# Kernel tuning notes

Measured on AMD Instinct MI355X. Metric: run time of the kernel, lower is better.

The kernel has to match this reference:

```python
import jax, jax.numpy as jnp
import numpy as np

B, S, E, H, D, R = 2, 2048, 1024, 16, 64, 16


def setup_inputs() -> dict:
    key = jax.random.key(0)
    ks = jax.random.split(key, 9)
    s = lambda k, shape, fan: jax.random.normal(k, shape, dtype=jnp.float32) / np.sqrt(fan)
    return {
        "x": jax.random.normal(ks[0], (B, S, E), dtype=jnp.float32),
        "Wq": s(ks[1], (H, E, D), E),
        "bq": jnp.zeros((H, D), jnp.float32),
        "Wk": s(ks[2], (H, E, D), E),
        "bk": jnp.zeros((H, D), jnp.float32),
        "Wvd": s(ks[3], (H, E, R), E),
        "bvd": jnp.zeros((H, R), jnp.float32),
        "Wvu": s(ks[4], (H, R, D), R),
        "bvu": jnp.zeros((H, D), jnp.float32),
    }


def reference(x, Wq, bq, Wk, bk, Wvd, bvd, Wvu, bvu):
    b, s, e = x.shape
    # per-head projections, vectorized over heads h
    q = jnp.einsum('bse,hed->bhsd', x, Wq) + bq[None, :, None, :]
    k = jnp.einsum('bse,hed->bhsd', x, Wk) + bk[None, :, None, :]
    # NOTE: original scales by sqrt(embedding_dimension), not head dim
    scores = jnp.einsum('bhsd,bhtd->bhst', q, k) / jnp.sqrt(jnp.float32(e))
    # original mask: masked_fill where key_idx < query_idx (anti-causal)
    qi = jnp.arange(s)[:, None]
    ki = jnp.arange(s)[None, :]
    scores = jnp.where(ki < qi, -jnp.inf, scores)
    att = jax.nn.softmax(scores, axis=-1)  # dropout p=0 (eval)
    # low-rank value: up(down(x))
    vd = jnp.einsum('bse,her->bhsr', x, Wvd) + bvd[None, :, None, :]
    v = jnp.einsum('bhsr,hrd->bhsd', vd, Wvu) + bvu[None, :, None, :]
    out = jnp.einsum('bhst,bhtd->bhsd', att, v)
    # concat heads along last dim (head order = stack order)
    return out.transpose(0, 2, 1, 3).reshape(b, s, -1)
```

## Files before the change

kernel.cpp:

```cpp
#include <hip/hip_runtime.h>
#include <stdint.h>

#define B_ 2
#define S_ 2048
#define E_ 1024
#define H_ 16
#define D_ 64
#define R_ 16

typedef short s16x8 __attribute__((ext_vector_type(8)));
typedef short s16x4 __attribute__((ext_vector_type(4)));
typedef float f32x4 __attribute__((ext_vector_type(4)));

__device__ __forceinline__ unsigned short f2bf(float f) {
  union { float f; unsigned u; } v; v.f = f;
  return (unsigned short)((v.u + 0x8000u) >> 16);
}

__device__ __forceinline__ void load_lds16(const void* g, void* l) {
  __builtin_amdgcn_global_load_lds(
      (__attribute__((address_space(1))) void*)(g),
      (__attribute__((address_space(3))) void*)(l), 16, 0, 0);
}


__global__ void k_cvt_x(const float* __restrict__ x, unsigned short* __restrict__ xb) {
  int i = (blockIdx.x * 256 + threadIdx.x) * 4;
  float4 v = *(const float4*)(x + i);
  ushort4 o;
  o.x = f2bf(v.x); o.y = f2bf(v.y); o.z = f2bf(v.z); o.w = f2bf(v.w);
  *(ushort4*)(xb + i) = o;
}

__global__ void k_prep_wqk(const float* __restrict__ Wq, const float* __restrict__ Wk,
                           unsigned short* __restrict__ Wt) {
  __shared__ float T[64][65];
  const int t = threadIdx.x;
  const int which = blockIdx.x >> 8;
  const int h = (blockIdx.x >> 4) & 15;
  const int et = blockIdx.x & 15;
  const float* src = (which ? Wk : Wq) + (h * E_ + et * 64) * D_;
#pragma unroll
  for (int pr = 0; pr < 4; ++pr) {
    const int row = pr * 16 + (t >> 4);
    const int col = (t & 15) * 4;
    float4 v = *(const float4*)(src + row * 64 + col);
    T[row][col] = v.x; T[row][col + 1] = v.y; T[row][col + 2] = v.z; T[row][col + 3] = v.w;
  }
  __syncthreads();
#pragma unroll
  for (int pr = 0; pr < 4; ++pr) {
    const int d = pr * 16 + (t >> 4);
    const int ec = (t & 15) * 4;
    ushort4 o;
    o.x = f2bf(T[ec][d]); o.y = f2bf(T[ec + 1][d]);
    o.z = f2bf(T[ec + 2][d]); o.w = f2bf(T[ec + 3][d]);
    *(ushort4*)(Wt + ((which << 10) + h * 64 + d) * 1024 + et * 64 + ec) = o;
  }
}

__global__ void k_prep_wv(const float* __restrict__ Wvd, const float* __restrict__ Wvu,
                          unsigned short* __restrict__ Wt) {
  const int idx = blockIdx.x * 256 + threadIdx.x;
  const int row = idx >> 10;
  const int e = idx & 1023;
  const int h = row >> 6, d = row & 63;
  const float4* wd4 = (const float4*)(Wvd + (h << 14) + e * 16);
  const float* wu = Wvu + h * R_ * D_ + d;
  float acc = 0.f;
#pragma unroll
  for (int r4 = 0; r4 < 4; ++r4) {
    float4 a = wd4[r4];
    acc += a.x * wu[(r4 * 4 + 0) * 64];
    acc += a.y * wu[(r4 * 4 + 1) * 64];
    acc += a.z * wu[(r4 * 4 + 2) * 64];
    acc += a.w * wu[(r4 * 4 + 3) * 64];
  }
  Wt[(2048 + row) * 1024 + e] = f2bf(acc);
}

__global__ void k_prep_b(const float* __restrict__ bq, const float* __restrict__ bk,
                         const float* __restrict__ bvd, const float* __restrict__ Wvu,
                         const float* __restrict__ bvu, float* __restrict__ ball) {
  int n = blockIdx.x * 256 + threadIdx.x;
  int which = n >> 10;
  int hd = n & 1023;
  int h = hd >> 6, d = hd & 63;
  float v;
  if (which == 0) v = bq[hd];
  else if (which == 1) v = bk[hd];
  else {
    v = bvu[hd];
#pragma unroll
    for (int r = 0; r < R_; ++r) v += bvd[h * R_ + r] * Wvu[(h * R_ + r) * D_ + d];
  }
  ball[n] = v;
}


__global__ __launch_bounds__(256, 2) void k_gemm_qkv(
    const unsigned short* __restrict__ X, const unsigned short* __restrict__ Wt,
    const float* __restrict__ ball,
    unsigned short* __restrict__ Qb, unsigned short* __restrict__ Kb,
    unsigned short* __restrict__ Vb) {
  __shared__ unsigned short As[128 * 32];
  __shared__ unsigned short Bs[128 * 32];
  const int tid = threadIdx.x;
  const int lane = tid & 63, wave = tid >> 6;
  const int quad = lane >> 4, l16 = lane & 15;
  const int mBase = blockIdx.y * 128, nBase = blockIdx.x * 128;
  const int wm = (wave & 1) * 64, wn = (wave >> 1) * 64;
  const int lrow = lane >> 2, lcol = (lane & 3) * 8;

  f32x4 acc[4][4];
#pragma unroll
  for (int mi = 0; mi < 4; ++mi)
#pragma unroll
    for (int ni = 0; ni < 4; ++ni) acc[mi][ni] = (f32x4){0.f, 0.f, 0.f, 0.f};

  for (int k0 = 0; k0 < E_; k0 += 32) {
#pragma unroll
    for (int i = 0; i < 2; ++i) {
      const int r0 = __builtin_amdgcn_readfirstlane((wave + i * 4) * 16);
      load_lds16(X + (mBase + r0 + lrow) * E_ + k0 + lcol, &As[r0 * 32]);
      load_lds16(Wt + (nBase + r0 + lrow) * E_ + k0 + lcol, &Bs[r0 * 32]);
    }
    __syncthreads();
    s16x8 af[4], bfr[4];
#pragma unroll
    for (int mi = 0; mi < 4; ++mi)
      af[mi] = *(const s16x8*)&As[(wm + mi * 16 + l16) * 32 + quad * 8];
#pragma unroll
    for (int ni = 0; ni < 4; ++ni)
      bfr[ni] = *(const s16x8*)&Bs[(wn + ni * 16 + l16) * 32 + quad * 8];
#pragma unroll
    for (int mi = 0; mi < 4; ++mi)
#pragma unroll
      for (int ni = 0; ni < 4; ++ni)
        acc[mi][ni] = __builtin_amdgcn_mfma_f32_16x16x32_bf16(af[mi], bfr[ni], acc[mi][ni], 0, 0, 0);
    __syncthreads();
  }

  const int which = nBase >> 10;
#pragma unroll
  for (int ni = 0; ni < 4; ++ni) {
    const int n = nBase + wn + ni * 16 + l16;
    const int nh = n & 1023;
    const int h = nh >> 6, d = nh & 63;
    const float bias = ball[n];
#pragma unroll
    for (int mi = 0; mi < 4; ++mi) {
      const int m0 = mBase + wm + mi * 16 + quad * 4;
      const int b = m0 >> 11;
      const int s = m0 & 2047;
      const int bh = b * H_ + h;
      if (which == 2) {
        ushort4 pk;
        pk.x = f2bf(acc[mi][ni][0] + bias);
        pk.y = f2bf(acc[mi][ni][1] + bias);
        pk.z = f2bf(acc[mi][ni][2] + bias);
        pk.w = f2bf(acc[mi][ni][3] + bias);
        *(ushort4*)(Vb + (bh * D_ + d) * S_ + s) = pk;
      } else {
        unsigned short* dst = (which == 0 ? Qb : Kb) + (bh * S_ + s) * D_ + d;
#pragma unroll
        for (int r = 0; r < 4; ++r) dst[r * D_] = f2bf(acc[mi][ni][r] + bias);
      }
    }
  }
}


__global__ __launch_bounds__(256, 2) void k_attn(
    const unsigned short* __restrict__ Qb, const unsigned short* __restrict__ Kb,
    const unsigned short* __restrict__ Vb, float* __restrict__ out) {
  __shared__ unsigned short Ks[2 * 64 * 32];
  __shared__ unsigned short Vs[2 * 64 * 32];
  __shared__ unsigned short Ps[4 * 2 * 16 * 36];
  const int tid = threadIdx.x;
  const int lane = tid & 63, wave = tid >> 6;
  const int quad = lane >> 4, l16 = lane & 15;
  const int bh = blockIdx.x & 31;
  const int qt = blockIdx.x >> 5;
  const int q0 = qt * 64;
  const int lrow = lane >> 2, lcol = (lane & 3) * 8;
  const float K1 = 1.44269504f / 32.f;
  const float K0 = -28.8539008f;

  s16x8 qf[2];
  {
    const unsigned short* qp = Qb + (bh * S_ + q0 + wave * 16 + l16) * D_ + quad * 8;
    qf[0] = *(const s16x8*)qp;
    qf[1] = *(const s16x8*)(qp + 32);
  }
  f32x4 o[4];
#pragma unroll
  for (int dc = 0; dc < 4; ++dc) o[dc] = (f32x4){0.f, 0.f, 0.f, 0.f};
  float l_acc[4] = {0.f, 0.f, 0.f, 0.f};

  unsigned short* myPs = &Ps[wave * 1152];

  for (int kt = qt; kt < S_ / 64; ++kt) {
    const int k0 = kt * 64;
    const int r0 = __builtin_amdgcn_readfirstlane(wave * 16);
#pragma unroll
    for (int hdc = 0; hdc < 2; ++hdc) {
      load_lds16(Kb + (bh * S_ + k0 + r0 + lrow) * D_ + hdc * 32 + lcol,
                 &Ks[hdc * 2048 + r0 * 32]);
      load_lds16(Vb + (bh * D_ + r0 + lrow) * S_ + k0 + hdc * 32 + lcol,
                 &Vs[hdc * 2048 + r0 * 32]);
    }
    __syncthreads();

    f32x4 sc[4];
#pragma unroll
    for (int tc = 0; tc < 4; ++tc) {
      f32x4 a = (f32x4){0.f, 0.f, 0.f, 0.f};
#pragma unroll
      for (int dc = 0; dc < 2; ++dc) {
        s16x8 kb = *(const s16x8*)&Ks[dc * 2048 + (tc * 16 + l16) * 32 + quad * 8];
        a = __builtin_amdgcn_mfma_f32_16x16x32_bf16(qf[dc], kb, a, 0, 0, 0);
      }
      sc[tc] = a;
    }

    if (kt == qt) {
#pragma unroll
      for (int tc = 0; tc < 4; ++tc)
#pragma unroll
        for (int r = 0; r < 4; ++r) {
          const int t = tc * 16 + l16;
          const int q = wave * 16 + quad * 4 + r;
          if (t < q) sc[tc][r] = -3.0e38f;
        }
    }

#pragma unroll
    for (int tc = 0; tc < 4; ++tc)
#pragma unroll
      for (int r = 0; r < 4; ++r) {
        float p = exp2f(fmaf(sc[tc][r], K1, K0));
        l_acc[r] += p;
        myPs[(tc >> 1) * 576 + (quad * 4 + r) * 36 + (tc & 1) * 16 + l16] = f2bf(p);
      }

#pragma unroll
    for (int dc = 0; dc < 4; ++dc) {
#pragma unroll
      for (int kc = 0; kc < 2; ++kc) {
        s16x4 plo = *(const s16x4*)&myPs[kc * 576 + l16 * 36 + quad * 8];
        s16x4 phi = *(const s16x4*)&myPs[kc * 576 + l16 * 36 + quad * 8 + 4];
        s16x8 pf = __builtin_shufflevector(plo, phi, 0, 1, 2, 3, 4, 5, 6, 7);
        s16x8 vb = *(const s16x8*)&Vs[kc * 2048 + (dc * 16 + l16) * 32 + quad * 8];
        o[dc] = __builtin_amdgcn_mfma_f32_16x16x32_bf16(pf, vb, o[dc], 0, 0, 0);
      }
    }
    __syncthreads();
  }

#pragma unroll
  for (int off = 1; off < 16; off <<= 1)
#pragma unroll
    for (int r = 0; r < 4; ++r) l_acc[r] += __shfl_xor(l_acc[r], off);
  float rinv[4];
#pragma unroll
  for (int r = 0; r < 4; ++r) rinv[r] = 1.f / l_acc[r];

  const int b = bh >> 4, h = bh & 15;
#pragma unroll
  for (int dc = 0; dc < 4; ++dc)
#pragma unroll
    for (int r = 0; r < 4; ++r) {
      const int s = q0 + wave * 16 + quad * 4 + r;
      out[(b * S_ + s) * (H_ * D_) + h * D_ + dc * 16 + l16] = o[dc][r] * rinv[r];
    }
}


extern "C" void kernel_launch(void* const* d_in, const int* in_sizes, int n_in,
                              void* d_out, int out_size, void* d_ws, size_t ws_size,
                              hipStream_t stream) {
  const float* x   = (const float*)d_in[0];
  const float* Wq  = (const float*)d_in[1];
  const float* bq  = (const float*)d_in[2];
  const float* Wk  = (const float*)d_in[3];
  const float* bk  = (const float*)d_in[4];
  const float* Wvd = (const float*)d_in[5];
  const float* bvd = (const float*)d_in[6];
  const float* Wvu = (const float*)d_in[7];
  const float* bvu = (const float*)d_in[8];
  float* out = (float*)d_out;

  char* ws = (char*)d_ws;
  unsigned short* xb   = (unsigned short*)(ws);
  unsigned short* Wt   = (unsigned short*)(ws + (8u << 20));
  float*          ball = (float*)(ws + (14u << 20));
  unsigned short* Qb   = (unsigned short*)(ws + (15u << 20));
  unsigned short* Kb   = (unsigned short*)(ws + (23u << 20));
  unsigned short* Vb   = (unsigned short*)(ws + (31u << 20));

  k_cvt_x<<<(B_ * S_ * E_ / 4) / 256, 256, 0, stream>>>(x, xb);
  k_prep_wqk<<<512, 256, 0, stream>>>(Wq, Wk, Wt);
  k_prep_wv<<<4096, 256, 0, stream>>>(Wvd, Wvu, Wt);
  k_prep_b<<<3072 / 256, 256, 0, stream>>>(bq, bk, bvd, Wvu, bvu, ball);
  k_gemm_qkv<<<dim3(3072 / 128, 4096 / 128), 256, 0, stream>>>(xb, Wt, ball, Qb, Kb, Vb);
  k_attn<<<(B_ * H_) * (S_ / 64), 256, 0, stream>>>(Qb, Kb, Vb, out);
}
```

Measured before the change: 184.9 us.

## Pair complementary query tiles per attention block, double-buffer K/V, merge prep kernels

Each attention block now handles two query tiles, pt and 31-pt. Under the anti-causal mask these have complementary key ranges, so every block does the same amount of work, and the grid halves to 512 blocks. The K/V LDS tiles are double-buffered, so the next tile's global-to-LDS load is issued before computing on the current one, and the trailing barrier is removed. The four preprocessing kernels (x conversion, Wq/Wk transpose, Wv fold, bias fold) are merged into one launch that dispatches on block index. This adds register pressure from holding two query states and doubles the K/V LDS footprint.

```diff
diff --git a/kernel.cpp b/kernel.cpp
--- a/kernel.cpp
+++ b/kernel.cpp
@@ -23,78 +23,77 @@
       (__attribute__((address_space(3))) void*)(l), 16, 0, 0);
 }
 
-
-__global__ void k_cvt_x(const float* __restrict__ x, unsigned short* __restrict__ xb) {
-  int i = (blockIdx.x * 256 + threadIdx.x) * 4;
-  float4 v = *(const float4*)(x + i);
-  ushort4 o;
-  o.x = f2bf(v.x); o.y = f2bf(v.y); o.z = f2bf(v.z); o.w = f2bf(v.w);
-  *(ushort4*)(xb + i) = o;
-}
-
-__global__ void k_prep_wqk(const float* __restrict__ Wq, const float* __restrict__ Wk,
-                           unsigned short* __restrict__ Wt) {
+__global__ void k_prep(const float* __restrict__ x,
+                       const float* __restrict__ Wq, const float* __restrict__ Wk,
+                       const float* __restrict__ Wvd, const float* __restrict__ Wvu,
+                       const float* __restrict__ bq, const float* __restrict__ bk,
+                       const float* __restrict__ bvd, const float* __restrict__ bvu,
+                       unsigned short* __restrict__ xb, unsigned short* __restrict__ Wt,
+                       float* __restrict__ ball) {
   __shared__ float T[64][65];
+  const int blk = blockIdx.x;
   const int t = threadIdx.x;
-  const int which = blockIdx.x >> 8;
-  const int h = (blockIdx.x >> 4) & 15;
-  const int et = blockIdx.x & 15;
-  const float* src = (which ? Wk : Wq) + (h * E_ + et * 64) * D_;
-#pragma unroll
-  for (int pr = 0; pr < 4; ++pr) {
-    const int row = pr * 16 + (t >> 4);
-    const int col = (t & 15) * 4;
-    float4 v = *(const float4*)(src + row * 64 + col);
-    T[row][col] = v.x; T[row][col + 1] = v.y; T[row][col + 2] = v.z; T[row][col + 3] = v.w;
-  }
-  __syncthreads();
-#pragma unroll
-  for (int pr = 0; pr < 4; ++pr) {
-    const int d = pr * 16 + (t >> 4);
-    const int ec = (t & 15) * 4;
+  if (blk < 4096) {
+    int i = (blk * 256 + t) * 4;
+    float4 v = *(const float4*)(x + i);
     ushort4 o;
-    o.x = f2bf(T[ec][d]); o.y = f2bf(T[ec + 1][d]);
-    o.z = f2bf(T[ec + 2][d]); o.w = f2bf(T[ec + 3][d]);
-    *(ushort4*)(Wt + ((which << 10) + h * 64 + d) * 1024 + et * 64 + ec) = o;
-  }
-}
-
-__global__ void k_prep_wv(const float* __restrict__ Wvd, const float* __restrict__ Wvu,
-                          unsigned short* __restrict__ Wt) {
-  const int idx = blockIdx.x * 256 + threadIdx.x;
-  const int row = idx >> 10;
-  const int e = idx & 1023;
-  const int h = row >> 6, d = row & 63;
-  const float4* wd4 = (const float4*)(Wvd + (h << 14) + e * 16);
-  const float* wu = Wvu + h * R_ * D_ + d;
-  float acc = 0.f;
-#pragma unroll
-  for (int r4 = 0; r4 < 4; ++r4) {
-    float4 a = wd4[r4];
-    acc += a.x * wu[(r4 * 4 + 0) * 64];
-    acc += a.y * wu[(r4 * 4 + 1) * 64];
-    acc += a.z * wu[(r4 * 4 + 2) * 64];
-    acc += a.w * wu[(r4 * 4 + 3) * 64];
-  }
-  Wt[(2048 + row) * 1024 + e] = f2bf(acc);
-}
-
-__global__ void k_prep_b(const float* __restrict__ bq, const float* __restrict__ bk,
-                         const float* __restrict__ bvd, const float* __restrict__ Wvu,
-                         const float* __restrict__ bvu, float* __restrict__ ball) {
-  int n = blockIdx.x * 256 + threadIdx.x;
-  int which = n >> 10;
-  int hd = n & 1023;
-  int h = hd >> 6, d = hd & 63;
-  float v;
-  if (which == 0) v = bq[hd];
-  else if (which == 1) v = bk[hd];
-  else {
-    v = bvu[hd];
-#pragma unroll
-    for (int r = 0; r < R_; ++r) v += bvd[h * R_ + r] * Wvu[(h * R_ + r) * D_ + d];
-  }
-  ball[n] = v;
+    o.x = f2bf(v.x); o.y = f2bf(v.y); o.z = f2bf(v.z); o.w = f2bf(v.w);
+    *(ushort4*)(xb + i) = o;
+  } else if (blk < 4608) {
+    const int bb = blk - 4096;
+    const int which = bb >> 8;
+    const int h = (bb >> 4) & 15;
+    const int et = bb & 15;
+    const float* src = (which ? Wk : Wq) + (h * E_ + et * 64) * D_;
+#pragma unroll
+    for (int pr = 0; pr < 4; ++pr) {
+      const int row = pr * 16 + (t >> 4);
+      const int col = (t & 15) * 4;
+      float4 v = *(const float4*)(src + row * 64 + col);
+      T[row][col] = v.x; T[row][col + 1] = v.y; T[row][col + 2] = v.z; T[row][col + 3] = v.w;
+    }
+    __syncthreads();
+#pragma unroll
+    for (int pr = 0; pr < 4; ++pr) {
+      const int d = pr * 16 + (t >> 4);
+      const int ec = (t & 15) * 4;
+      ushort4 o;
+      o.x = f2bf(T[ec][d]); o.y = f2bf(T[ec + 1][d]);
+      o.z = f2bf(T[ec + 2][d]); o.w = f2bf(T[ec + 3][d]);
+      *(ushort4*)(Wt + ((which << 10) + h * 64 + d) * 1024 + et * 64 + ec) = o;
+    }
+  } else if (blk < 8704) {
+    const int idx = (blk - 4608) * 256 + t;
+    const int row = idx >> 10;
+    const int e = idx & 1023;
+    const int h = row >> 6, d = row & 63;
+    const float4* wd4 = (const float4*)(Wvd + (h << 14) + e * 16);
+    const float* wu = Wvu + h * R_ * D_ + d;
+    float acc = 0.f;
+#pragma unroll
+    for (int r4 = 0; r4 < 4; ++r4) {
+      float4 a = wd4[r4];
+      acc += a.x * wu[(r4 * 4 + 0) * 64];
+      acc += a.y * wu[(r4 * 4 + 1) * 64];
+      acc += a.z * wu[(r4 * 4 + 2) * 64];
+      acc += a.w * wu[(r4 * 4 + 3) * 64];
+    }
+    Wt[(2048 + row) * 1024 + e] = f2bf(acc);
+  } else {
+    int n = (blk - 8704) * 256 + t;
+    int which = n >> 10;
+    int hd = n & 1023;
+    int h = hd >> 6, d = hd & 63;
+    float v;
+    if (which == 0) v = bq[hd];
+    else if (which == 1) v = bk[hd];
+    else {
+      v = bvu[hd];
+#pragma unroll
+      for (int r = 0; r < R_; ++r) v += bvd[h * R_ + r] * Wvu[(h * R_ + r) * D_ + d];
+    }
+    ball[n] = v;
+  }
 }
 
 
@@ -171,109 +170,138 @@
 }
 
 
+struct QState {
+  s16x8 qf[2];
+  f32x4 o[4];
+  float l[4];
+};
+
+__device__ __forceinline__ void attn_tile(
+    QState& st, const unsigned short* Ksb, const unsigned short* Vsb,
+    unsigned short* myPs, int quad, int l16, int wave, bool diag) {
+  const float K1 = 1.44269504f / 32.f;
+  const float K0 = -28.8539008f;
+  f32x4 sc[4];
+#pragma unroll
+  for (int tc = 0; tc < 4; ++tc) {
+    f32x4 a = (f32x4){0.f, 0.f, 0.f, 0.f};
+#pragma unroll
+    for (int dc = 0; dc < 2; ++dc) {
+      s16x8 kb = *(const s16x8*)&Ksb[dc * 2048 + (tc * 16 + l16) * 32 + quad * 8];
+      a = __builtin_amdgcn_mfma_f32_16x16x32_bf16(st.qf[dc], kb, a, 0, 0, 0);
+    }
+    sc[tc] = a;
+  }
+  if (diag) {
+#pragma unroll
+    for (int tc = 0; tc < 4; ++tc)
+#pragma unroll
+      for (int r = 0; r < 4; ++r) {
+        const int t = tc * 16 + l16;
+        const int q = wave * 16 + quad * 4 + r;
+        if (t < q) sc[tc][r] = -3.0e38f;
+      }
+  }
+#pragma unroll
+  for (int tc = 0; tc < 4; ++tc)
+#pragma unroll
+    for (int r = 0; r < 4; ++r) {
+      float p = exp2f(fmaf(sc[tc][r], K1, K0));
+      st.l[r] += p;
+      myPs[(tc >> 1) * 576 + (quad * 4 + r) * 36 + (tc & 1) * 16 + l16] = f2bf(p);
+    }
+#pragma unroll
+  for (int dc = 0; dc < 4; ++dc) {
+#pragma unroll
+    for (int kc = 0; kc < 2; ++kc) {
+      s16x4 plo = *(const s16x4*)&myPs[kc * 576 + l16 * 36 + quad * 8];
+      s16x4 phi = *(const s16x4*)&myPs[kc * 576 + l16 * 36 + quad * 8 + 4];
+      s16x8 pf = __builtin_shufflevector(plo, phi, 0, 1, 2, 3, 4, 5, 6, 7);
+      s16x8 vb = *(const s16x8*)&Vsb[kc * 2048 + (dc * 16 + l16) * 32 + quad * 8];
+      st.o[dc] = __builtin_amdgcn_mfma_f32_16x16x32_bf16(pf, vb, st.o[dc], 0, 0, 0);
+    }
+  }
+}
+
 __global__ __launch_bounds__(256, 2) void k_attn(
     const unsigned short* __restrict__ Qb, const unsigned short* __restrict__ Kb,
     const unsigned short* __restrict__ Vb, float* __restrict__ out) {
-  __shared__ unsigned short Ks[2 * 64 * 32];
-  __shared__ unsigned short Vs[2 * 64 * 32];
+  __shared__ unsigned short Ks[2][2 * 64 * 32];
+  __shared__ unsigned short Vs[2][2 * 64 * 32];
   __shared__ unsigned short Ps[4 * 2 * 16 * 36];
   const int tid = threadIdx.x;
   const int lane = tid & 63, wave = tid >> 6;
   const int quad = lane >> 4, l16 = lane & 15;
   const int bh = blockIdx.x & 31;
-  const int qt = blockIdx.x >> 5;
-  const int q0 = qt * 64;
+  const int pt = blockIdx.x >> 5;
+  const int qa = pt, qb = 31 - pt;
   const int lrow = lane >> 2, lcol = (lane & 3) * 8;
-  const float K1 = 1.44269504f / 32.f;
-  const float K0 = -28.8539008f;
-
-  s16x8 qf[2];
+  const int r0 = __builtin_amdgcn_readfirstlane(wave * 16);
+
+  QState A, Bt;
   {
-    const unsigned short* qp = Qb + (bh * S_ + q0 + wave * 16 + l16) * D_ + quad * 8;
-    qf[0] = *(const s16x8*)qp;
-    qf[1] = *(const s16x8*)(qp + 32);
-  }
-  f32x4 o[4];
-#pragma unroll
-  for (int dc = 0; dc < 4; ++dc) o[dc] = (f32x4){0.f, 0.f, 0.f, 0.f};
-  float l_acc[4] = {0.f, 0.f, 0.f, 0.f};
+    const unsigned short* qp = Qb + (bh * S_ + qa * 64 + wave * 16 + l16) * D_ + quad * 8;
+    A.qf[0] = *(const s16x8*)qp;
+    A.qf[1] = *(const s16x8*)(qp + 32);
+    const unsigned short* qp2 = Qb + (bh * S_ + qb * 64 + wave * 16 + l16) * D_ + quad * 8;
+    Bt.qf[0] = *(const s16x8*)qp2;
+    Bt.qf[1] = *(const s16x8*)(qp2 + 32);
+  }
+#pragma unroll
+  for (int dc = 0; dc < 4; ++dc) {
+    A.o[dc] = (f32x4){0.f, 0.f, 0.f, 0.f};
+    Bt.o[dc] = (f32x4){0.f, 0.f, 0.f, 0.f};
+  }
+#pragma unroll
+  for (int r = 0; r < 4; ++r) { A.l[r] = 0.f; Bt.l[r] = 0.f; }
 
   unsigned short* myPs = &Ps[wave * 1152];
 
-  for (int kt = qt; kt < S_ / 64; ++kt) {
-    const int k0 = kt * 64;
-    const int r0 = __builtin_amdgcn_readfirstlane(wave * 16);
-#pragma unroll
-    for (int hdc = 0; hdc < 2; ++hdc) {
-      load_lds16(Kb + (bh * S_ + k0 + r0 + lrow) * D_ + hdc * 32 + lcol,
-                 &Ks[hdc * 2048 + r0 * 32]);
-      load_lds16(Vb + (bh * D_ + r0 + lrow) * S_ + k0 + hdc * 32 + lcol,
-                 &Vs[hdc * 2048 + r0 * 32]);
-    }
+#pragma unroll
+  for (int hdc = 0; hdc < 2; ++hdc) {
+    load_lds16(Kb + (bh * S_ + qa * 64 + r0 + lrow) * D_ + hdc * 32 + lcol,
+               &Ks[0][hdc * 2048 + r0 * 32]);
+    load_lds16(Vb + (bh * D_ + r0 + lrow) * S_ + qa * 64 + hdc * 32 + lcol,
+               &Vs[0][hdc * 2048 + r0 * 32]);
+  }
+
+  int buf = 0;
+  for (int kt = qa; kt < 32; ++kt) {
     __syncthreads();
-
-    f32x4 sc[4];
-#pragma unroll
-    for (int tc = 0; tc < 4; ++tc) {
-      f32x4 a = (f32x4){0.f, 0.f, 0.f, 0.f};
-#pragma unroll
-      for (int dc = 0; dc < 2; ++dc) {
-        s16x8 kb = *(const s16x8*)&Ks[dc * 2048 + (tc * 16 + l16) * 32 + quad * 8];
-        a = __builtin_amdgcn_mfma_f32_16x16x32_bf16(qf[dc], kb, a, 0, 0, 0);
+    if (kt + 1 < 32) {
+      const int k0n = (kt + 1) * 64;
+#pragma unroll
+      for (int hdc = 0; hdc < 2; ++hdc) {
+        load_lds16(Kb + (bh * S_ + k0n + r0 + lrow) * D_ + hdc * 32 + lcol,
+                   &Ks[buf ^ 1][hdc * 2048 + r0 * 32]);
+        load_lds16(Vb + (bh * D_ + r0 + lrow) * S_ + k0n + hdc * 32 + lcol,
+                   &Vs[buf ^ 1][hdc * 2048 + r0 * 32]);
       }
-      sc[tc] = a;
-    }
-
-    if (kt == qt) {
-#pragma unroll
-      for (int tc = 0; tc < 4; ++tc)
-#pragma unroll
-        for (int r = 0; r < 4; ++r) {
-          const int t = tc * 16 + l16;
-          const int q = wave * 16 + quad * 4 + r;
-          if (t < q) sc[tc][r] = -3.0e38f;
-        }
-    }
-
-#pragma unroll
-    for (int tc = 0; tc < 4; ++tc)
-#pragma unroll
-      for (int r = 0; r < 4; ++r) {
-        float p = exp2f(fmaf(sc[tc][r], K1, K0));
-        l_acc[r] += p;
-        myPs[(tc >> 1) * 576 + (quad * 4 + r) * 36 + (tc & 1) * 16 + l16] = f2bf(p);
-      }
-
+    }
+    attn_tile(A, Ks[buf], Vs[buf], myPs, quad, l16, wave, kt == qa);
+    if (kt >= qb) attn_tile(Bt, Ks[buf], Vs[buf], myPs, quad, l16, wave, kt == qb);
+    buf ^= 1;
+  }
+
+#pragma unroll
+  for (int off = 1; off < 16; off <<= 1)
+#pragma unroll
+    for (int r = 0; r < 4; ++r) {
+      A.l[r] += __shfl_xor(A.l[r], off);
+      Bt.l[r] += __shfl_xor(Bt.l[r], off);
+    }
+  const int b = bh >> 4, h = bh & 15;
+#pragma unroll
+  for (int r = 0; r < 4; ++r) {
+    const float ra = 1.f / A.l[r], rb = 1.f / Bt.l[r];
+    const int sa = qa * 64 + wave * 16 + quad * 4 + r;
+    const int sb = qb * 64 + wave * 16 + quad * 4 + r;
 #pragma unroll
     for (int dc = 0; dc < 4; ++dc) {
-#pragma unroll
-      for (int kc = 0; kc < 2; ++kc) {
-        s16x4 plo = *(const s16x4*)&myPs[kc * 576 + l16 * 36 + quad * 8];
-        s16x4 phi = *(const s16x4*)&myPs[kc * 576 + l16 * 36 + quad * 8 + 4];
-        s16x8 pf = __builtin_shufflevector(plo, phi, 0, 1, 2, 3, 4, 5, 6, 7);
-        s16x8 vb = *(const s16x8*)&Vs[kc * 2048 + (dc * 16 + l16) * 32 + quad * 8];
-        o[dc] = __builtin_amdgcn_mfma_f32_16x16x32_bf16(pf, vb, o[dc], 0, 0, 0);
-      }
-    }
-    __syncthreads();
-  }
-
-#pragma unroll
-  for (int off = 1; off < 16; off <<= 1)
-#pragma unroll
-    for (int r = 0; r < 4; ++r) l_acc[r] += __shfl_xor(l_acc[r], off);
-  float rinv[4];
-#pragma unroll
-  for (int r = 0; r < 4; ++r) rinv[r] = 1.f / l_acc[r];
-
-  const int b = bh >> 4, h = bh & 15;
-#pragma unroll
-  for (int dc = 0; dc < 4; ++dc)
-#pragma unroll
-    for (int r = 0; r < 4; ++r) {
-      const int s = q0 + wave * 16 + quad * 4 + r;
-      out[(b * S_ + s) * (H_ * D_) + h * D_ + dc * 16 + l16] = o[dc][r] * rinv[r];
-    }
+      out[(b * S_ + sa) * (H_ * D_) + h * D_ + dc * 16 + l16] = A.o[dc][r] * ra;
+      out[(b * S_ + sb) * (H_ * D_) + h * D_ + dc * 16 + l16] = Bt.o[dc][r] * rb;
+    }
+  }
 }
 
 
@@ -299,10 +327,7 @@
   unsigned short* Kb   = (unsigned short*)(ws + (23u << 20));
   unsigned short* Vb   = (unsigned short*)(ws + (31u << 20));
 
-  k_cvt_x<<<(B_ * S_ * E_ / 4) / 256, 256, 0, stream>>>(x, xb);
-  k_prep_wqk<<<512, 256, 0, stream>>>(Wq, Wk, Wt);
-  k_prep_wv<<<4096, 256, 0, stream>>>(Wvd, Wvu, Wt);
-  k_prep_b<<<3072 / 256, 256, 0, stream>>>(bq, bk, bvd, Wvu, bvu, ball);
+  k_prep<<<8716, 256, 0, stream>>>(x, Wq, Wk, Wvd, Wvu, bq, bk, bvd, bvu, xb, Wt, ball);
   k_gemm_qkv<<<dim3(3072 / 128, 4096 / 128), 256, 0, stream>>>(xb, Wt, ball, Qb, Kb, Vb);
-  k_attn<<<(B_ * H_) * (S_ / 64), 256, 0, stream>>>(Qb, Kb, Vb, out);
-}
+  k_attn<<<512, 256, 0, stream>>>(Qb, Kb, Vb, out);
+}
```

Result: faster. 173.3 us (-6.3%).
